# Kernel tuning notes

Hardware: AMD Instinct MI355X
Metric: run time of the kernel (lower is better)

The kernel has to match this reference:

```python
import jax, jax.numpy as jnp
import numpy as np

N_QUBITS = 12
LAYERS = 2
BATCH = 1024


def _apply_1q(state, gate, q):
    # state: [B] + [2]*n (wire 0 = leading qubit axis); gate: [2,2] or [B,2,2]
    axis = 1 + q
    st = jnp.moveaxis(state, axis, -1)
    if gate.ndim == 2:
        st = jnp.einsum('ij,...j->...i', gate, st)
    else:  # batched gate (angle depends on the input sample)
        st = jnp.einsum('bij,b...j->b...i', gate, st)
    return jnp.moveaxis(st, -1, axis)


def _apply_cnot(state, c, t):
    # flip target axis on the control=1 slice
    ca, ta = 1 + c, 1 + t
    a0 = jnp.take(state, 0, axis=ca)
    a1 = jnp.take(state, 1, axis=ca)
    ta2 = ta - 1 if ta > ca else ta
    a1 = jnp.flip(a1, axis=ta2)
    return jnp.stack([a0, a1], axis=ca)


def _rx(a):
    # a: [B] -> gate [B,2,2]
    h = 0.5 * a
    c = jnp.cos(h).astype(jnp.complex64)
    s = (-1j) * jnp.sin(h).astype(jnp.complex64)
    return jnp.stack([jnp.stack([c, s], -1), jnp.stack([s, c], -1)], -2)


def _ry(a):
    h = 0.5 * a
    c = jnp.cos(h).astype(jnp.complex64)
    s = jnp.sin(h).astype(jnp.complex64)
    return jnp.stack([jnp.stack([c, -s], -1), jnp.stack([s, c], -1)], -2)


def _rz(a):
    h = 0.5 * a
    e0 = jnp.exp(-1j * h.astype(jnp.complex64))
    e1 = jnp.exp(1j * h.astype(jnp.complex64))
    z = jnp.zeros_like(e0)
    return jnp.stack([jnp.stack([e0, z], -1), jnp.stack([z, e1], -1)], -2)


def setup_inputs() -> dict:
    key = jax.random.key(0)
    k1, k2 = jax.random.split(key)
    x = jax.random.normal(k1, (BATCH, N_QUBITS), dtype=jnp.float32)
    theta = jax.random.normal(k2, (LAYERS, N_QUBITS, 2), dtype=jnp.float32)
    lam = jnp.ones((LAYERS, N_QUBITS), dtype=jnp.float32)
    return {"x": x, "theta": theta, "lam": lam}


def reference(x, theta, lam):
    B = x.shape[0]
    n = N_QUBITS
    # |0...0> state, batched: [B] + [2]*n
    state = jnp.zeros((B,) + (2,) * n, dtype=jnp.complex64)
    state = state.at[(slice(None),) + (0,) * n].set(1.0)
    for l in range(LAYERS):
        for q in range(n):
            state = _apply_1q(state, _rx(lam[l, q] * x[:, q]), q)
        for q in range(n):
            state = _apply_cnot(state, q, (q + 1) % n)
        for q in range(n):
            state = _apply_1q(state, _ry(theta[l, q, 0]), q)
            state = _apply_1q(state, _rz(theta[l, q, 1]), q)
    probs = state.real ** 2 + state.imag ** 2  # [B] + [2]*n
    zs = []
    for q in range(n):
        axes = tuple(i for i in range(1, n + 1) if i != 1 + q)
        p = jnp.sum(probs, axis=axes)  # [B, 2]
        zs.append(p[:, 0] - p[:, 1])   # <Z_q>
    return jnp.stack(zs, axis=1)  # [B, n_qubits]
```

## Files before the change

### kernel.cpp

```cpp
#include <hip/hip_runtime.h>
#include <math.h>

#define NQ 12
#define TPB 256


__device__ __forceinline__ float2 pk_mul(float2 a, float2 b) {
    float2 d;
    asm("v_pk_mul_f32 %0, %1, %2" : "=v"(d) : "v"(a), "v"(b));
    return d;
}
__device__ __forceinline__ float2 pk_fma(float2 a, float2 b, float2 c) {
    float2 d;
    asm("v_pk_fma_f32 %0, %1, %2, %3" : "=v"(d) : "v"(a), "v"(b), "v"(c));
    return d;
}
__device__ __forceinline__ float2 pk_fma_sw0(float2 a, float2 b, float2 c) {
    float2 d;
    asm("v_pk_fma_f32 %0, %1, %2, %3 op_sel:[1,0,0] op_sel_hi:[0,1,1]"
        : "=v"(d) : "v"(a), "v"(b), "v"(c));
    return d;
}
__device__ __forceinline__ float2 pk_fma_n1(float2 a, float2 b, float2 c) {
    float2 d;
    asm("v_pk_fma_f32 %0, %1, %2, %3 neg_lo:[0,1,0] neg_hi:[0,1,0]"
        : "=v"(d) : "v"(a), "v"(b), "v"(c));
    return d;
}
__device__ __forceinline__ float2 pk_fma_sw0n1(float2 a, float2 b, float2 c) {
    float2 d;
    asm("v_pk_fma_f32 %0, %1, %2, %3 op_sel:[1,0,0] op_sel_hi:[0,1,1] "
        "neg_lo:[0,1,0] neg_hi:[0,1,0]"
        : "=v"(d) : "v"(a), "v"(b), "v"(c));
    return d;
}

#define FOR_PAIRS4(RB, ...) do {                                      \
    const int msk_ = 1 << (RB);                                       \
    _Pragma("unroll")                                                 \
    for (int h_ = 0; h_ < 8; ++h_) {                                  \
        const int i0 = ((h_ & ~(msk_ - 1)) << 1) | (h_ & (msk_ - 1)); \
        const int i1 = i0 | msk_;                                     \
        __VA_ARGS__;                                                  \
    } } while (0)

#define ADDR_A(r) (VA ^ (257 * (r)))
#define ADDR_B(r) (VB ^ (17 * (r)))
#define ADDR_C(r) (VC ^ (r))

#define LOCAL_X(AS, AD) do {                                          \
    _Pragma("unroll")                                                 \
    for (int r_ = 0; r_ < 16; ++r_) S[AS(r_)] = v[r_];                \
    _Pragma("unroll")                                                 \
    for (int r_ = 0; r_ < 16; ++r_) v[r_] = S[AD(r_)];                \
  } while (0)

#define M_GATE(q, RB) do {                                                  \
        const float2 ar = gm[q][0];                                         \
        const float2 ai = gm[q][1];                                         \
        const float2 br = gm[q][2];                                         \
        const float2 bi = gm[q][3];                                         \
        FOR_PAIRS4(RB,                                                      \
            const float2 v0 = v[i0];                                        \
            const float2 v1 = v[i1];                                        \
            float2 n0 = pk_mul(v0, ar);                                     \
            n0 = pk_fma_sw0(v0, ai, n0);                                    \
            n0 = pk_fma_n1(v1, br, n0);                                     \
            n0 = pk_fma_sw0(v1, bi, n0);                                    \
            float2 n1 = pk_mul(v0, br);                                     \
            n1 = pk_fma_sw0(v0, bi, n1);                                    \
            n1 = pk_fma(v1, ar, n1);                                        \
            n1 = pk_fma_sw0n1(v1, ai, n1);                                  \
            v[i0] = n0; v[i1] = n1;                                         \
        );                                                                  \
    } while (0)

#define RY_GATE(q, RB) do {                                                 \
        const float2 c2 = gy[q][0];                                         \
        const float2 s2 = gy[q][1];                                         \
        FOR_PAIRS4(RB,                                                      \
            float2 n0 = pk_fma_n1(v[i1], s2, pk_mul(v[i0], c2));            \
            float2 n1 = pk_fma(v[i0], s2, pk_mul(v[i1], c2));               \
            v[i0] = n0; v[i1] = n1;                                         \
        );                                                                  \
    } while (0)

#define M_PHASE(QB)  do { _Pragma("unroll")                                 \
    for (int d_ = 0; d_ < 4; ++d_) M_GATE((QB) + d_, 3 - d_); } while (0)
#define RY_PHASE(QB) do { _Pragma("unroll")                                 \
    for (int d_ = 0; d_ < 4; ++d_) RY_GATE((QB) + d_, 3 - d_); } while (0)

__global__ __launch_bounds__(TPB, 4) void vqc_kernel(
    const float* __restrict__ x,
    const float* __restrict__ th,
    const float* __restrict__ lm,
    float* __restrict__ out)
{
    __shared__ float2 S[4096];
    __shared__ float2 gm[12][4];
    __shared__ float2 gy[12][2];
    __shared__ float2 coI[12];
    __shared__ float red[4 * 12];

    const int b = blockIdx.x;
    const int t = threadIdx.x;
    const int l = t & 63;
    const int w = t >> 6;

    const int kC = (t ^ (t >> 4)) & 15;
    const int VA = (t & 0xF0) | kC;
    const int VB = ((t >> 4) << 8) | kC;
    const int VC = (t << 4) | kC;
    int Ft;
    {
        int yt = t ^ (t >> 1); yt ^= yt >> 2; yt ^= yt >> 4; yt ^= yt >> 8;
        int pt = (yt & 0x7FF) | ((__popc(t) & 1) << 11);
        Ft = (pt & ~15) | ((pt ^ (pt >> 4) ^ (pt >> 8)) & 15);
    }

    if (t < 12) {
        float h = 0.5f * lm[t] * x[b * NQ + t];
        float c, s; __sincosf(h, &s, &c);
        coI[t] = make_float2(c, s);
    } else if (t < 24) {
        int q = t - 12;
        float h = 0.5f * th[24 + 2 * q];
        float c, s; __sincosf(h, &s, &c);
        gy[q][0] = make_float2(c, c);
        gy[q][1] = make_float2(s, s);
    } else if (t < 36) {
        int q = t - 24;
        float ha = 0.5f * lm[12 + q] * x[b * NQ + q];
        float hy = 0.5f * th[2 * q];
        float hz = 0.5f * th[2 * q + 1];
        float ca, sa, cy, sy, cz, sz;
        __sincosf(ha, &sa, &ca);
        __sincosf(hy, &sy, &cy);
        __sincosf(hz, &sz, &cz);
        float ax = ca*cy*cz + sa*sy*sz;
        float ay = -(ca*cy*sz + sa*sy*cz);
        float bx = ca*sy*cz - sa*cy*sz;
        float by = ca*sy*sz - sa*cy*cz;
        gm[q][0] = make_float2(ax, ax);
        gm[q][1] = make_float2(-ay, ay);
        gm[q][2] = make_float2(bx, bx);
        gm[q][3] = make_float2(-by, by);
    }
    __syncthreads();

    float2 v[16];

    {
        const int g = (t ^ (t >> 1)) & 0x3F;
        float Pt = 1.0f;
#pragma unroll
        for (int m = 0; m < 6; ++m) {
            float2 cs = coI[7 - m];
            Pt *= ((g >> m) & 1) ? cs.y : cs.x;
        }
        const int ct = __popc(g);
        const int t0 = t & 1, t7 = (t >> 7) & 1;
        const int e1 = ((t >> 6) ^ (t >> 7)) & 1;
        float2 q11 = coI[11], q10 = coI[10], q9 = coI[9],
               q8 = coI[8], q1 = coI[1], q0 = coI[0];
        const float u8  = t0 ? q8.y : q8.x;
        const float u8n = t0 ? q8.x : q8.y;
        const float u1  = e1 ? q1.y : q1.x;
        const float u1n = e1 ? q1.x : q1.y;
        const float u0  = t7 ? q0.y : q0.x;
        const float u0n = t7 ? q0.x : q0.y;
#pragma unroll
        for (int r = 0; r < 16; ++r) {
            const int r0 = r & 1, r1 = (r >> 1) & 1, r2 = (r >> 2) & 1,
                      r3 = (r >> 3) & 1;
            const int b11 = r0 ^ r1, b10 = r1 ^ r2, b9 = r2 ^ r3;
            float m = Pt * (b11 ? q11.y : q11.x) * (b10 ? q10.y : q10.x)
                         * (b9 ? q9.y : q9.x) * (r3 ? u8n : u8)
                         * (r0 ? u1n : u1) * (r0 ? u0n : u0);
            int k = (ct + b11 + b10 + b9 + (r3 ^ t0) + (r0 ^ e1) + (r0 ^ t7)) & 3;
            v[r].x = (k == 0) ? m : ((k == 2) ? -m : 0.0f);
            v[r].y = (k == 3) ? m : ((k == 1) ? -m : 0.0f);
        }
    }

    M_PHASE(8);
    LOCAL_X(ADDR_C, ADDR_B);
    M_PHASE(4);
#pragma unroll
    for (int r = 0; r < 16; ++r) S[ADDR_B(r)] = v[r];
    __syncthreads();
#pragma unroll
    for (int r = 0; r < 16; ++r) v[r] = S[ADDR_A(r)];
    M_PHASE(0);

    __syncthreads();
#pragma unroll
    for (int r = 0; r < 16; ++r) {
        const int jr = r << 8;
        int yr = jr ^ (jr >> 1); yr ^= yr >> 2; yr ^= yr >> 4; yr ^= yr >> 8;
        const int pr = (yr & 0x7FF) | (((__popc(jr) ^ (jr >> 11)) & 1) << 11);
        const int Gr = (pr & ~15) | ((pr ^ (pr >> 4) ^ (pr >> 8)) & 15);
        S[Ft ^ Gr] = v[r];
    }
    __syncthreads();
#pragma unroll
    for (int r = 0; r < 16; ++r) v[r] = S[ADDR_A(r)];

    RY_PHASE(0);
#pragma unroll
    for (int r = 0; r < 16; ++r) S[ADDR_A(r)] = v[r];
    __syncthreads();
#pragma unroll
    for (int r = 0; r < 16; ++r) v[r] = S[ADDR_B(r)];
    RY_PHASE(4);
    LOCAL_X(ADDR_B, ADDR_C);
    RY_PHASE(8);

    float p[16];
#pragma unroll
    for (int r = 0; r < 16; ++r)
        p[r] = fmaf(v[r].x, v[r].x, v[r].y * v[r].y);
    float sA[8], dA[8];
#pragma unroll
    for (int k = 0; k < 8; ++k) {
        sA[k] = p[2 * k] + p[2 * k + 1];
        dA[k] = p[2 * k] - p[2 * k + 1];
    }
    float z11 = ((dA[0] + dA[1]) + (dA[2] + dA[3]))
              + ((dA[4] + dA[5]) + (dA[6] + dA[7]));
    float sC[4], dC[4];
#pragma unroll
    for (int k = 0; k < 4; ++k) {
        sC[k] = sA[2 * k] + sA[2 * k + 1];
        dC[k] = sA[2 * k] - sA[2 * k + 1];
    }
    float z10 = (dC[0] + dC[1]) + (dC[2] + dC[3]);
    float e0 = sC[0] + sC[1], f0 = sC[0] - sC[1];
    float e1s = sC[2] + sC[3], f1 = sC[2] - sC[3];
    float vals[5];
    vals[0] = e0 + e1s;
    vals[1] = e0 - e1s;
    vals[2] = f0 + f1;
    vals[3] = z10;
    vals[4] = z11;

#pragma unroll
    for (int k = 0; k < 6; ++k) {
        const float sgn = ((l >> k) & 1) ? -1.f : 1.f;
#pragma unroll
        for (int m = 0; m < 5; ++m) {
            float tmp = __shfl_xor(vals[m], 1 << k, 64);
            vals[m] = fmaf(sgn, vals[m], tmp);
        }
    }
    if (l == 0) {
        red[w * 12 + 0]  = vals[0];
        red[w * 12 + 8]  = vals[1];
        red[w * 12 + 9]  = vals[2];
        red[w * 12 + 10] = vals[3];
        red[w * 12 + 11] = vals[4];
    } else if (__popc(l) == 1) {
        int q = 8 - __ffs(l);
        red[w * 12 + q] = vals[0];
    }
    __syncthreads();
    if (t < NQ) {
        float acc = 0.f;
#pragma unroll
        for (int ww = 0; ww < 4; ++ww) {
            if (t < 2) {
                float pv = red[ww * 12 + 0];
                acc += ((ww >> (1 - t)) & 1) ? -pv : pv;
            } else {
                acc += red[ww * 12 + t];
            }
        }
        out[b * NQ + t] = acc;
    }
}

extern "C" void kernel_launch(void* const* d_in, const int* in_sizes, int n_in,
                              void* d_out, int out_size, void* d_ws, size_t ws_size,
                              hipStream_t stream) {
    const int B = in_sizes[0] / NQ;
    vqc_kernel<<<B, TPB, 0, stream>>>((const float*)d_in[0],
                                      (const float*)d_in[1],
                                      (const float*)d_in[2],
                                      (float*)d_out);
}
```

Baseline: 73.29 us.

## Redesign shared-memory state layout for 128-bit gathers in qubit transposes

Replaces the XOR-swizzled per-element shared-memory exchange with a new layout where each thread's 16 amplitudes come back as eight float4 (128-bit) LDS reads. Stores use new swizzled bases and the CNOT permutation mapping is rewritten to match. Gate coefficients are also loaded as float4, and the gate order within each phase is reversed to follow the new register-bit assignment. An extra __syncthreads is added before each cross-thread store because stores now overwrite data other threads may still be reading. This trades fewer LDS instructions for extra barriers and a possible rise in bank conflicts on the stores.

New measurement: 74.43 us. About the same (+1.5%).

```diff
diff --git a/kernel.cpp b/kernel.cpp
--- a/kernel.cpp
+++ b/kernel.cpp
@@ -44,22 +44,35 @@
         __VA_ARGS__;                                                  \
     } } while (0)
 
-#define ADDR_A(r) (VA ^ (257 * (r)))
-#define ADDR_B(r) (VB ^ (17 * (r)))
-#define ADDR_C(r) (VC ^ (r))
-
-#define LOCAL_X(AS, AD) do {                                          \
+#define GATHER do {                                                   \
     _Pragma("unroll")                                                 \
-    for (int r_ = 0; r_ < 16; ++r_) S[AS(r_)] = v[r_];                \
+    for (int k_ = 0; k_ < 8; ++k_) {                                  \
+        float4 g_ = F4[RB4 ^ k_];                                     \
+        v[2 * k_]     = make_float2(g_.x, g_.y);                      \
+        v[2 * k_ + 1] = make_float2(g_.z, g_.w);                      \
+    } } while (0)
+
+#define STORE_LOCAL do {                                              \
     _Pragma("unroll")                                                 \
-    for (int r_ = 0; r_ < 16; ++r_) v[r_] = S[AD(r_)];                \
-  } while (0)
+    for (int r_ = 0; r_ < 16; ++r_)                                   \
+        S[base1 ^ ((r_ << 4) | ((r_ & 7) << 1))] = v[r_];             \
+    } while (0)
+
+#define STORE_CROSS do {                                              \
+    _Pragma("unroll")                                                 \
+    for (int r_ = 0; r_ < 16; ++r_)                                   \
+        S[base2 + (r_ << 8)] = v[r_];                                 \
+    } while (0)
+
+#define CFENCE asm volatile("" ::: "memory")
 
 #define M_GATE(q, RB) do {                                                  \
-        const float2 ar = gm[q][0];                                         \
-        const float2 ai = gm[q][1];                                         \
-        const float2 br = gm[q][2];                                         \
-        const float2 bi = gm[q][3];                                         \
+        const float4 gA_ = gm4[2 * (q)];                                    \
+        const float4 gB_ = gm4[2 * (q) + 1];                                \
+        const float2 ar = make_float2(gA_.x, gA_.y);                        \
+        const float2 ai = make_float2(gA_.z, gA_.w);                        \
+        const float2 br = make_float2(gB_.x, gB_.y);                        \
+        const float2 bi = make_float2(gB_.z, gB_.w);                        \
         FOR_PAIRS4(RB,                                                      \
             const float2 v0 = v[i0];                                        \
             const float2 v1 = v[i1];                                        \
@@ -76,8 +89,9 @@
     } while (0)
 
 #define RY_GATE(q, RB) do {                                                 \
-        const float2 c2 = gy[q][0];                                         \
-        const float2 s2 = gy[q][1];                                         \
+        const float4 gY_ = gy4[q];                                          \
+        const float2 c2 = make_float2(gY_.x, gY_.y);                        \
+        const float2 s2 = make_float2(gY_.z, gY_.w);                        \
         FOR_PAIRS4(RB,                                                      \
             float2 n0 = pk_fma_n1(v[i1], s2, pk_mul(v[i0], c2));            \
             float2 n1 = pk_fma(v[i0], s2, pk_mul(v[i1], c2));               \
@@ -86,9 +100,9 @@
     } while (0)
 
 #define M_PHASE(QB)  do { _Pragma("unroll")                                 \
-    for (int d_ = 0; d_ < 4; ++d_) M_GATE((QB) + d_, 3 - d_); } while (0)
+    for (int d_ = 3; d_ >= 0; --d_) M_GATE((QB) + d_, 3 - d_); } while (0)
 #define RY_PHASE(QB) do { _Pragma("unroll")                                 \
-    for (int d_ = 0; d_ < 4; ++d_) RY_GATE((QB) + d_, 3 - d_); } while (0)
+    for (int d_ = 3; d_ >= 0; --d_) RY_GATE((QB) + d_, 3 - d_); } while (0)
 
 __global__ __launch_bounds__(TPB, 4) void vqc_kernel(
     const float* __restrict__ x,
@@ -96,26 +110,30 @@
     const float* __restrict__ lm,
     float* __restrict__ out)
 {
-    __shared__ float2 S[4096];
-    __shared__ float2 gm[12][4];
-    __shared__ float2 gy[12][2];
+    __shared__ alignas(16) float2 S[4096];
+    __shared__ alignas(16) float2 gm[12][4];
+    __shared__ alignas(16) float2 gy[12][2];
     __shared__ float2 coI[12];
     __shared__ float red[4 * 12];
+
+    float4* F4 = reinterpret_cast<float4*>(S);
+    const float4* gm4 = reinterpret_cast<const float4*>(gm);
+    const float4* gy4 = reinterpret_cast<const float4*>(gy);
 
     const int b = blockIdx.x;
     const int t = threadIdx.x;
     const int l = t & 63;
     const int w = t >> 6;
 
-    const int kC = (t ^ (t >> 4)) & 15;
-    const int VA = (t & 0xF0) | kC;
-    const int VB = ((t >> 4) << 8) | kC;
-    const int VC = (t << 4) | kC;
-    int Ft;
+    const int RB4   = (t << 3) | (t & 7);
+    const int base1 = ((t & 0xF0) << 4) | (t & 15);
+    const int base2 = ((t & 15) << 4)
+                    | ((((t >> 4) & 15) ^ ((t & 7) << 1)) & 15);
+    int Et3;
     {
         int yt = t ^ (t >> 1); yt ^= yt >> 2; yt ^= yt >> 4; yt ^= yt >> 8;
         int pt = (yt & 0x7FF) | ((__popc(t) & 1) << 11);
-        Ft = (pt & ~15) | ((pt ^ (pt >> 4) ^ (pt >> 8)) & 15);
+        Et3 = ((pt & 0xFF) << 4) | ((((pt >> 8) & 15) ^ ((pt & 7) << 1)) & 15);
     }
 
     if (t < 12) {
@@ -184,13 +202,12 @@
     }
 
     M_PHASE(8);
-    LOCAL_X(ADDR_C, ADDR_B);
+    STORE_LOCAL; CFENCE; GATHER;
     M_PHASE(4);
-#pragma unroll
-    for (int r = 0; r < 16; ++r) S[ADDR_B(r)] = v[r];
-    __syncthreads();
-#pragma unroll
-    for (int r = 0; r < 16; ++r) v[r] = S[ADDR_A(r)];
+    __syncthreads();
+    STORE_CROSS;
+    __syncthreads();
+    GATHER;
     M_PHASE(0);
 
     __syncthreads();
@@ -199,21 +216,20 @@
         const int jr = r << 8;
         int yr = jr ^ (jr >> 1); yr ^= yr >> 2; yr ^= yr >> 4; yr ^= yr >> 8;
         const int pr = (yr & 0x7FF) | (((__popc(jr) ^ (jr >> 11)) & 1) << 11);
-        const int Gr = (pr & ~15) | ((pr ^ (pr >> 4) ^ (pr >> 8)) & 15);
-        S[Ft ^ Gr] = v[r];
-    }
-    __syncthreads();
-#pragma unroll
-    for (int r = 0; r < 16; ++r) v[r] = S[ADDR_A(r)];
+        const int Gr = ((pr & 0xFF) << 4)
+                     | ((((pr >> 8) & 15) ^ ((pr & 7) << 1)) & 15);
+        S[Et3 ^ Gr] = v[r];
+    }
+    __syncthreads();
+    GATHER;
 
     RY_PHASE(0);
-#pragma unroll
-    for (int r = 0; r < 16; ++r) S[ADDR_A(r)] = v[r];
-    __syncthreads();
-#pragma unroll
-    for (int r = 0; r < 16; ++r) v[r] = S[ADDR_B(r)];
+    __syncthreads();
+    STORE_CROSS;
+    __syncthreads();
+    GATHER;
     RY_PHASE(4);
-    LOCAL_X(ADDR_B, ADDR_C);
+    STORE_LOCAL; CFENCE; GATHER;
     RY_PHASE(8);
 
     float p[16];
```

## Process two batch samples per block with interleaved state vectors

Applied to the files above, without the earlier changes.

Each block now simulates two samples at once, keeping two 16-amplitude register sets and two shared-memory state buffers, and interleaves their gate work. The aim is more instruction-level parallelism and fewer barriers per sample, at the cost of doubled registers and LDS per block, half as many blocks (512), and lower launch-bounds occupancy. Grid launch assumes an even batch size.

New measurement: 75.93 us. 1.04x slower.

```diff
diff --git a/kernel.cpp b/kernel.cpp
--- a/kernel.cpp
+++ b/kernel.cpp
@@ -48,64 +48,80 @@
 #define ADDR_B(r) (VB ^ (17 * (r)))
 #define ADDR_C(r) (VC ^ (r))
 
-#define LOCAL_X(AS, AD) do {                                          \
+#define CFENCE asm volatile("" ::: "memory")
+
+#define LOCAL_X2(AS, AD) do {                                         \
     _Pragma("unroll")                                                 \
-    for (int r_ = 0; r_ < 16; ++r_) S[AS(r_)] = v[r_];                \
+    for (int r_ = 0; r_ < 16; ++r_) {                                 \
+        S0[AS(r_)] = v0[r_]; S1[AS(r_)] = v1[r_];                     \
+    }                                                                 \
+    CFENCE;                                                           \
     _Pragma("unroll")                                                 \
-    for (int r_ = 0; r_ < 16; ++r_) v[r_] = S[AD(r_)];                \
-  } while (0)
-
-#define M_GATE(q, RB) do {                                                  \
-        const float2 ar = gm[q][0];                                         \
-        const float2 ai = gm[q][1];                                         \
-        const float2 br = gm[q][2];                                         \
-        const float2 bi = gm[q][3];                                         \
+    for (int r_ = 0; r_ < 16; ++r_) {                                 \
+        v0[r_] = S0[AD(r_)]; v1[r_] = S1[AD(r_)];                     \
+    } } while (0)
+
+#define M_GATE(GM, q, RB, V) do {                                           \
+        const float2 ar = GM[q][0];                                         \
+        const float2 ai = GM[q][1];                                         \
+        const float2 br = GM[q][2];                                         \
+        const float2 bi = GM[q][3];                                         \
         FOR_PAIRS4(RB,                                                      \
-            const float2 v0 = v[i0];                                        \
-            const float2 v1 = v[i1];                                        \
-            float2 n0 = pk_mul(v0, ar);                                     \
-            n0 = pk_fma_sw0(v0, ai, n0);                                    \
-            n0 = pk_fma_n1(v1, br, n0);                                     \
-            n0 = pk_fma_sw0(v1, bi, n0);                                    \
-            float2 n1 = pk_mul(v0, br);                                     \
-            n1 = pk_fma_sw0(v0, bi, n1);                                    \
-            n1 = pk_fma(v1, ar, n1);                                        \
-            n1 = pk_fma_sw0n1(v1, ai, n1);                                  \
-            v[i0] = n0; v[i1] = n1;                                         \
+            const float2 a0 = V[i0];                                        \
+            const float2 a1 = V[i1];                                        \
+            float2 n0 = pk_mul(a0, ar);                                     \
+            n0 = pk_fma_sw0(a0, ai, n0);                                    \
+            n0 = pk_fma_n1(a1, br, n0);                                     \
+            n0 = pk_fma_sw0(a1, bi, n0);                                    \
+            float2 n1 = pk_mul(a0, br);                                     \
+            n1 = pk_fma_sw0(a0, bi, n1);                                    \
+            n1 = pk_fma(a1, ar, n1);                                        \
+            n1 = pk_fma_sw0n1(a1, ai, n1);                                  \
+            V[i0] = n0; V[i1] = n1;                                         \
         );                                                                  \
     } while (0)
 
-#define RY_GATE(q, RB) do {                                                 \
+#define RY_GATE(q, RB, V) do {                                              \
         const float2 c2 = gy[q][0];                                         \
         const float2 s2 = gy[q][1];                                         \
         FOR_PAIRS4(RB,                                                      \
-            float2 n0 = pk_fma_n1(v[i1], s2, pk_mul(v[i0], c2));            \
-            float2 n1 = pk_fma(v[i0], s2, pk_mul(v[i1], c2));               \
-            v[i0] = n0; v[i1] = n1;                                         \
+            float2 n0 = pk_fma_n1(V[i1], s2, pk_mul(V[i0], c2));            \
+            float2 n1 = pk_fma(V[i0], s2, pk_mul(V[i1], c2));               \
+            V[i0] = n0; V[i1] = n1;                                         \
         );                                                                  \
     } while (0)
 
-#define M_PHASE(QB)  do { _Pragma("unroll")                                 \
-    for (int d_ = 0; d_ < 4; ++d_) M_GATE((QB) + d_, 3 - d_); } while (0)
-#define RY_PHASE(QB) do { _Pragma("unroll")                                 \
-    for (int d_ = 0; d_ < 4; ++d_) RY_GATE((QB) + d_, 3 - d_); } while (0)
-
-__global__ __launch_bounds__(TPB, 4) void vqc_kernel(
+#define M_PHASE2(QB)  do { _Pragma("unroll")                                \
+    for (int d_ = 0; d_ < 4; ++d_) {                                        \
+        M_GATE(gmP0, (QB) + d_, 3 - d_, v0);                                \
+        M_GATE(gmP1, (QB) + d_, 3 - d_, v1);                                \
+    } } while (0)
+#define RY_PHASE2(QB) do { _Pragma("unroll")                                \
+    for (int d_ = 0; d_ < 4; ++d_) {                                        \
+        RY_GATE((QB) + d_, 3 - d_, v0);                                     \
+        RY_GATE((QB) + d_, 3 - d_, v1);                                     \
+    } } while (0)
+
+__global__ __launch_bounds__(TPB, 2) void vqc_kernel(
     const float* __restrict__ x,
     const float* __restrict__ th,
     const float* __restrict__ lm,
     float* __restrict__ out)
 {
-    __shared__ float2 S[4096];
-    __shared__ float2 gm[12][4];
+    __shared__ alignas(16) float2 S0[4096];
+    __shared__ alignas(16) float2 S1[4096];
+    __shared__ float2 gm[2][12][4];
     __shared__ float2 gy[12][2];
-    __shared__ float2 coI[12];
-    __shared__ float red[4 * 12];
+    __shared__ float2 coI[2][12];
+    __shared__ float red[2][4 * 12];
 
     const int b = blockIdx.x;
     const int t = threadIdx.x;
     const int l = t & 63;
     const int w = t >> 6;
+
+    const float2 (*gmP0)[4] = gm[0];
+    const float2 (*gmP1)[4] = gm[1];
 
     const int kC = (t ^ (t >> 4)) & 15;
     const int VA = (t & 0xF0) | kC;
@@ -118,51 +134,58 @@
         Ft = (pt & ~15) | ((pt ^ (pt >> 4) ^ (pt >> 8)) & 15);
     }
 
-    if (t < 12) {
-        float h = 0.5f * lm[t] * x[b * NQ + t];
-        float c, s; __sincosf(h, &s, &c);
-        coI[t] = make_float2(c, s);
-    } else if (t < 24) {
-        int q = t - 12;
-        float h = 0.5f * th[24 + 2 * q];
-        float c, s; __sincosf(h, &s, &c);
-        gy[q][0] = make_float2(c, c);
-        gy[q][1] = make_float2(s, s);
-    } else if (t < 36) {
-        int q = t - 24;
-        float ha = 0.5f * lm[12 + q] * x[b * NQ + q];
-        float hy = 0.5f * th[2 * q];
-        float hz = 0.5f * th[2 * q + 1];
-        float ca, sa, cy, sy, cz, sz;
-        __sincosf(ha, &sa, &ca);
-        __sincosf(hy, &sy, &cy);
-        __sincosf(hz, &sz, &cz);
-        float ax = ca*cy*cz + sa*sy*sz;
-        float ay = -(ca*cy*sz + sa*sy*cz);
-        float bx = ca*sy*cz - sa*cy*sz;
-        float by = ca*sy*sz - sa*cy*cz;
-        gm[q][0] = make_float2(ax, ax);
-        gm[q][1] = make_float2(-ay, ay);
-        gm[q][2] = make_float2(bx, bx);
-        gm[q][3] = make_float2(-by, by);
-    }
-    __syncthreads();
-
-    float2 v[16];
-
-    {
+    if (t < 72) {
+        const int s = t / 36;
+        const int u = t - 36 * s;
+        const int bb = 2 * b + s;
+        if (u < 12) {
+            float h = 0.5f * lm[u] * x[bb * NQ + u];
+            float c, sn; __sincosf(h, &sn, &c);
+            coI[s][u] = make_float2(c, sn);
+        } else if (u < 24) {
+            if (s == 0) {
+                int q = u - 12;
+                float h = 0.5f * th[24 + 2 * q];
+                float c, sn; __sincosf(h, &sn, &c);
+                gy[q][0] = make_float2(c, c);
+                gy[q][1] = make_float2(sn, sn);
+            }
+        } else {
+            int q = u - 24;
+            float ha = 0.5f * lm[12 + q] * x[bb * NQ + q];
+            float hy = 0.5f * th[2 * q];
+            float hz = 0.5f * th[2 * q + 1];
+            float ca, sa, cy, sy, cz, sz;
+            __sincosf(ha, &sa, &ca);
+            __sincosf(hy, &sy, &cy);
+            __sincosf(hz, &sz, &cz);
+            float ax = ca*cy*cz + sa*sy*sz;
+            float ay = -(ca*cy*sz + sa*sy*cz);
+            float bx = ca*sy*cz - sa*cy*sz;
+            float by = ca*sy*sz - sa*cy*cz;
+            gm[s][q][0] = make_float2(ax, ax);
+            gm[s][q][1] = make_float2(-ay, ay);
+            gm[s][q][2] = make_float2(bx, bx);
+            gm[s][q][3] = make_float2(-by, by);
+        }
+    }
+    __syncthreads();
+
+    float2 v0[16], v1[16];
+
+    auto init_state = [&](const float2* coIs, float2* v) {
         const int g = (t ^ (t >> 1)) & 0x3F;
         float Pt = 1.0f;
 #pragma unroll
         for (int m = 0; m < 6; ++m) {
-            float2 cs = coI[7 - m];
+            float2 cs = coIs[7 - m];
             Pt *= ((g >> m) & 1) ? cs.y : cs.x;
         }
         const int ct = __popc(g);
         const int t0 = t & 1, t7 = (t >> 7) & 1;
         const int e1 = ((t >> 6) ^ (t >> 7)) & 1;
-        float2 q11 = coI[11], q10 = coI[10], q9 = coI[9],
-               q8 = coI[8], q1 = coI[1], q0 = coI[0];
+        float2 q11 = coIs[11], q10 = coIs[10], q9 = coIs[9],
+               q8 = coIs[8], q1 = coIs[1], q0 = coIs[0];
         const float u8  = t0 ? q8.y : q8.x;
         const float u8n = t0 ? q8.x : q8.y;
         const float u1  = e1 ? q1.y : q1.x;
@@ -181,17 +204,23 @@
             v[r].x = (k == 0) ? m : ((k == 2) ? -m : 0.0f);
             v[r].y = (k == 3) ? m : ((k == 1) ? -m : 0.0f);
         }
-    }
-
-    M_PHASE(8);
-    LOCAL_X(ADDR_C, ADDR_B);
-    M_PHASE(4);
-#pragma unroll
-    for (int r = 0; r < 16; ++r) S[ADDR_B(r)] = v[r];
-    __syncthreads();
-#pragma unroll
-    for (int r = 0; r < 16; ++r) v[r] = S[ADDR_A(r)];
-    M_PHASE(0);
+    };
+    init_state(coI[0], v0);
+    init_state(coI[1], v1);
+
+    M_PHASE2(8);
+    LOCAL_X2(ADDR_C, ADDR_B);
+    M_PHASE2(4);
+#pragma unroll
+    for (int r = 0; r < 16; ++r) {
+        S0[ADDR_B(r)] = v0[r]; S1[ADDR_B(r)] = v1[r];
+    }
+    __syncthreads();
+#pragma unroll
+    for (int r = 0; r < 16; ++r) {
+        v0[r] = S0[ADDR_A(r)]; v1[r] = S1[ADDR_A(r)];
+    }
+    M_PHASE2(0);
 
     __syncthreads();
 #pragma unroll
@@ -200,82 +229,98 @@
         int yr = jr ^ (jr >> 1); yr ^= yr >> 2; yr ^= yr >> 4; yr ^= yr >> 8;
         const int pr = (yr & 0x7FF) | (((__popc(jr) ^ (jr >> 11)) & 1) << 11);
         const int Gr = (pr & ~15) | ((pr ^ (pr >> 4) ^ (pr >> 8)) & 15);
-        S[Ft ^ Gr] = v[r];
-    }
-    __syncthreads();
-#pragma unroll
-    for (int r = 0; r < 16; ++r) v[r] = S[ADDR_A(r)];
-
-    RY_PHASE(0);
-#pragma unroll
-    for (int r = 0; r < 16; ++r) S[ADDR_A(r)] = v[r];
-    __syncthreads();
-#pragma unroll
-    for (int r = 0; r < 16; ++r) v[r] = S[ADDR_B(r)];
-    RY_PHASE(4);
-    LOCAL_X(ADDR_B, ADDR_C);
-    RY_PHASE(8);
-
-    float p[16];
-#pragma unroll
-    for (int r = 0; r < 16; ++r)
-        p[r] = fmaf(v[r].x, v[r].x, v[r].y * v[r].y);
-    float sA[8], dA[8];
-#pragma unroll
-    for (int k = 0; k < 8; ++k) {
-        sA[k] = p[2 * k] + p[2 * k + 1];
-        dA[k] = p[2 * k] - p[2 * k + 1];
-    }
-    float z11 = ((dA[0] + dA[1]) + (dA[2] + dA[3]))
-              + ((dA[4] + dA[5]) + (dA[6] + dA[7]));
-    float sC[4], dC[4];
-#pragma unroll
-    for (int k = 0; k < 4; ++k) {
-        sC[k] = sA[2 * k] + sA[2 * k + 1];
-        dC[k] = sA[2 * k] - sA[2 * k + 1];
-    }
-    float z10 = (dC[0] + dC[1]) + (dC[2] + dC[3]);
-    float e0 = sC[0] + sC[1], f0 = sC[0] - sC[1];
-    float e1s = sC[2] + sC[3], f1 = sC[2] - sC[3];
-    float vals[5];
-    vals[0] = e0 + e1s;
-    vals[1] = e0 - e1s;
-    vals[2] = f0 + f1;
-    vals[3] = z10;
-    vals[4] = z11;
+        S0[Ft ^ Gr] = v0[r]; S1[Ft ^ Gr] = v1[r];
+    }
+    __syncthreads();
+#pragma unroll
+    for (int r = 0; r < 16; ++r) {
+        v0[r] = S0[ADDR_A(r)]; v1[r] = S1[ADDR_A(r)];
+    }
+
+    RY_PHASE2(0);
+#pragma unroll
+    for (int r = 0; r < 16; ++r) {
+        S0[ADDR_A(r)] = v0[r]; S1[ADDR_A(r)] = v1[r];
+    }
+    __syncthreads();
+#pragma unroll
+    for (int r = 0; r < 16; ++r) {
+        v0[r] = S0[ADDR_B(r)]; v1[r] = S1[ADDR_B(r)];
+    }
+    RY_PHASE2(4);
+    LOCAL_X2(ADDR_B, ADDR_C);
+    RY_PHASE2(8);
+
+    float vals[10];
+    auto reduce5 = [&](const float2* v, float* va) {
+        float p[16];
+#pragma unroll
+        for (int r = 0; r < 16; ++r)
+            p[r] = fmaf(v[r].x, v[r].x, v[r].y * v[r].y);
+        float sA[8], dA[8];
+#pragma unroll
+        for (int k = 0; k < 8; ++k) {
+            sA[k] = p[2 * k] + p[2 * k + 1];
+            dA[k] = p[2 * k] - p[2 * k + 1];
+        }
+        float z11 = ((dA[0] + dA[1]) + (dA[2] + dA[3]))
+                  + ((dA[4] + dA[5]) + (dA[6] + dA[7]));
+        float sC[4], dC[4];
+#pragma unroll
+        for (int k = 0; k < 4; ++k) {
+            sC[k] = sA[2 * k] + sA[2 * k + 1];
+            dC[k] = sA[2 * k] - sA[2 * k + 1];
+        }
+        float z10 = (dC[0] + dC[1]) + (dC[2] + dC[3]);
+        float e0 = sC[0] + sC[1], f0 = sC[0] - sC[1];
+        float e1s = sC[2] + sC[3], f1 = sC[2] - sC[3];
+        va[0] = e0 + e1s;
+        va[1] = e0 - e1s;
+        va[2] = f0 + f1;
+        va[3] = z10;
+        va[4] = z11;
+    };
+    reduce5(v0, vals);
+    reduce5(v1, vals + 5);
 
 #pragma unroll
     for (int k = 0; k < 6; ++k) {
         const float sgn = ((l >> k) & 1) ? -1.f : 1.f;
 #pragma unroll
-        for (int m = 0; m < 5; ++m) {
+        for (int m = 0; m < 10; ++m) {
             float tmp = __shfl_xor(vals[m], 1 << k, 64);
             vals[m] = fmaf(sgn, vals[m], tmp);
         }
     }
     if (l == 0) {
-        red[w * 12 + 0]  = vals[0];
-        red[w * 12 + 8]  = vals[1];
-        red[w * 12 + 9]  = vals[2];
-        red[w * 12 + 10] = vals[3];
-        red[w * 12 + 11] = vals[4];
+#pragma unroll
+        for (int s = 0; s < 2; ++s) {
+            red[s][w * 12 + 0]  = vals[5 * s + 0];
+            red[s][w * 12 + 8]  = vals[5 * s + 1];
+            red[s][w * 12 + 9]  = vals[5 * s + 2];
+            red[s][w * 12 + 10] = vals[5 * s + 3];
+            red[s][w * 12 + 11] = vals[5 * s + 4];
+        }
     } else if (__popc(l) == 1) {
         int q = 8 - __ffs(l);
-        red[w * 12 + q] = vals[0];
-    }
-    __syncthreads();
-    if (t < NQ) {
+        red[0][w * 12 + q] = vals[0];
+        red[1][w * 12 + q] = vals[5];
+    }
+    __syncthreads();
+    if (t < 2 * NQ) {
+        const int s = t / NQ;
+        const int q = t - NQ * s;
         float acc = 0.f;
 #pragma unroll
         for (int ww = 0; ww < 4; ++ww) {
-            if (t < 2) {
-                float pv = red[ww * 12 + 0];
-                acc += ((ww >> (1 - t)) & 1) ? -pv : pv;
+            if (q < 2) {
+                float pv = red[s][ww * 12 + 0];
+                acc += ((ww >> (1 - q)) & 1) ? -pv : pv;
             } else {
-                acc += red[ww * 12 + t];
+                acc += red[s][ww * 12 + q];
             }
         }
-        out[b * NQ + t] = acc;
+        out[(2 * b + s) * NQ + q] = acc;
     }
 }
 
@@ -283,8 +328,8 @@
                               void* d_out, int out_size, void* d_ws, size_t ws_size,
                               hipStream_t stream) {
     const int B = in_sizes[0] / NQ;
-    vqc_kernel<<<B, TPB, 0, stream>>>((const float*)d_in[0],
-                                      (const float*)d_in[1],
-                                      (const float*)d_in[2],
-                                      (float*)d_out);
-}
+    vqc_kernel<<<B / 2, TPB, 0, stream>>>((const float*)d_in[0],
+                                          (const float*)d_in[1],
+                                          (const float*)d_in[2],
+                                          (float*)d_out);
+}
```

## Process four batch samples per block in a loop

Applied to the files above, without the earlier changes.

Each block now loops over four batch samples, and the launch uses a quarter as many blocks. This amortises block launch overhead and reuses the resident block across samples. It also adds a compiler memory fence inside the local shared-memory exchange and renames temporaries in the gate macro. The trade-off is fewer blocks: 256 blocks on 256 CUs leaves roughly one block per CU with no latency hiding, and each sample is processed serially. Sample loads and trig setup are not overlapped with the previous sample's compute. B is also assumed to be divisible by 4.

New measurement: 94.48 us. 1.29x slower.

```diff
diff --git a/kernel.cpp b/kernel.cpp
--- a/kernel.cpp
+++ b/kernel.cpp
@@ -48,9 +48,12 @@
 #define ADDR_B(r) (VB ^ (17 * (r)))
 #define ADDR_C(r) (VC ^ (r))
 
+#define CFENCE asm volatile("" ::: "memory")
+
 #define LOCAL_X(AS, AD) do {                                          \
     _Pragma("unroll")                                                 \
     for (int r_ = 0; r_ < 16; ++r_) S[AS(r_)] = v[r_];                \
+    CFENCE;                                                           \
     _Pragma("unroll")                                                 \
     for (int r_ = 0; r_ < 16; ++r_) v[r_] = S[AD(r_)];                \
   } while (0)
@@ -61,16 +64,16 @@
         const float2 br = gm[q][2];                                         \
         const float2 bi = gm[q][3];                                         \
         FOR_PAIRS4(RB,                                                      \
-            const float2 v0 = v[i0];                                        \
-            const float2 v1 = v[i1];                                        \
-            float2 n0 = pk_mul(v0, ar);                                     \
-            n0 = pk_fma_sw0(v0, ai, n0);                                    \
-            n0 = pk_fma_n1(v1, br, n0);                                     \
-            n0 = pk_fma_sw0(v1, bi, n0);                                    \
-            float2 n1 = pk_mul(v0, br);                                     \
-            n1 = pk_fma_sw0(v0, bi, n1);                                    \
-            n1 = pk_fma(v1, ar, n1);                                        \
-            n1 = pk_fma_sw0n1(v1, ai, n1);                                  \
+            const float2 a0 = v[i0];                                        \
+            const float2 a1 = v[i1];                                        \
+            float2 n0 = pk_mul(a0, ar);                                     \
+            n0 = pk_fma_sw0(a0, ai, n0);                                    \
+            n0 = pk_fma_n1(a1, br, n0);                                     \
+            n0 = pk_fma_sw0(a1, bi, n0);                                    \
+            float2 n1 = pk_mul(a0, br);                                     \
+            n1 = pk_fma_sw0(a0, bi, n1);                                    \
+            n1 = pk_fma(a1, ar, n1);                                        \
+            n1 = pk_fma_sw0n1(a1, ai, n1);                                  \
             v[i0] = n0; v[i1] = n1;                                         \
         );                                                                  \
     } while (0)
@@ -102,7 +105,6 @@
     __shared__ float2 coI[12];
     __shared__ float red[4 * 12];
 
-    const int b = blockIdx.x;
     const int t = threadIdx.x;
     const int l = t & 63;
     const int w = t >> 6;
@@ -118,164 +120,169 @@
         Ft = (pt & ~15) | ((pt ^ (pt >> 4) ^ (pt >> 8)) & 15);
     }
 
-    if (t < 12) {
-        float h = 0.5f * lm[t] * x[b * NQ + t];
-        float c, s; __sincosf(h, &s, &c);
-        coI[t] = make_float2(c, s);
-    } else if (t < 24) {
-        int q = t - 12;
-        float h = 0.5f * th[24 + 2 * q];
-        float c, s; __sincosf(h, &s, &c);
-        gy[q][0] = make_float2(c, c);
-        gy[q][1] = make_float2(s, s);
-    } else if (t < 36) {
-        int q = t - 24;
-        float ha = 0.5f * lm[12 + q] * x[b * NQ + q];
-        float hy = 0.5f * th[2 * q];
-        float hz = 0.5f * th[2 * q + 1];
-        float ca, sa, cy, sy, cz, sz;
-        __sincosf(ha, &sa, &ca);
-        __sincosf(hy, &sy, &cy);
-        __sincosf(hz, &sz, &cz);
-        float ax = ca*cy*cz + sa*sy*sz;
-        float ay = -(ca*cy*sz + sa*sy*cz);
-        float bx = ca*sy*cz - sa*cy*sz;
-        float by = ca*sy*sz - sa*cy*cz;
-        gm[q][0] = make_float2(ax, ax);
-        gm[q][1] = make_float2(-ay, ay);
-        gm[q][2] = make_float2(bx, bx);
-        gm[q][3] = make_float2(-by, by);
-    }
-    __syncthreads();
-
-    float2 v[16];
-
-    {
-        const int g = (t ^ (t >> 1)) & 0x3F;
-        float Pt = 1.0f;
-#pragma unroll
-        for (int m = 0; m < 6; ++m) {
-            float2 cs = coI[7 - m];
-            Pt *= ((g >> m) & 1) ? cs.y : cs.x;
-        }
-        const int ct = __popc(g);
-        const int t0 = t & 1, t7 = (t >> 7) & 1;
-        const int e1 = ((t >> 6) ^ (t >> 7)) & 1;
-        float2 q11 = coI[11], q10 = coI[10], q9 = coI[9],
-               q8 = coI[8], q1 = coI[1], q0 = coI[0];
-        const float u8  = t0 ? q8.y : q8.x;
-        const float u8n = t0 ? q8.x : q8.y;
-        const float u1  = e1 ? q1.y : q1.x;
-        const float u1n = e1 ? q1.x : q1.y;
-        const float u0  = t7 ? q0.y : q0.x;
-        const float u0n = t7 ? q0.x : q0.y;
+    for (int s = 0; s < 4; ++s) {
+        const int b = blockIdx.x * 4 + s;
+
+        if (t < 12) {
+            float h = 0.5f * lm[t] * x[b * NQ + t];
+            float c, sn; __sincosf(h, &sn, &c);
+            coI[t] = make_float2(c, sn);
+        } else if (t < 24) {
+            int q = t - 12;
+            float h = 0.5f * th[24 + 2 * q];
+            float c, sn; __sincosf(h, &sn, &c);
+            gy[q][0] = make_float2(c, c);
+            gy[q][1] = make_float2(sn, sn);
+        } else if (t < 36) {
+            int q = t - 24;
+            float ha = 0.5f * lm[12 + q] * x[b * NQ + q];
+            float hy = 0.5f * th[2 * q];
+            float hz = 0.5f * th[2 * q + 1];
+            float ca, sa, cy, sy, cz, sz;
+            __sincosf(ha, &sa, &ca);
+            __sincosf(hy, &sy, &cy);
+            __sincosf(hz, &sz, &cz);
+            float ax = ca*cy*cz + sa*sy*sz;
+            float ay = -(ca*cy*sz + sa*sy*cz);
+            float bx = ca*sy*cz - sa*cy*sz;
+            float by = ca*sy*sz - sa*cy*cz;
+            gm[q][0] = make_float2(ax, ax);
+            gm[q][1] = make_float2(-ay, ay);
+            gm[q][2] = make_float2(bx, bx);
+            gm[q][3] = make_float2(-by, by);
+        }
+        __syncthreads();
+
+        float2 v[16];
+
+        {
+            const int g = (t ^ (t >> 1)) & 0x3F;
+            float Pt = 1.0f;
+#pragma unroll
+            for (int m = 0; m < 6; ++m) {
+                float2 cs = coI[7 - m];
+                Pt *= ((g >> m) & 1) ? cs.y : cs.x;
+            }
+            const int ct = __popc(g);
+            const int t0 = t & 1, t7 = (t >> 7) & 1;
+            const int e1 = ((t >> 6) ^ (t >> 7)) & 1;
+            float2 q11 = coI[11], q10 = coI[10], q9 = coI[9],
+                   q8 = coI[8], q1 = coI[1], q0 = coI[0];
+            const float u8  = t0 ? q8.y : q8.x;
+            const float u8n = t0 ? q8.x : q8.y;
+            const float u1  = e1 ? q1.y : q1.x;
+            const float u1n = e1 ? q1.x : q1.y;
+            const float u0  = t7 ? q0.y : q0.x;
+            const float u0n = t7 ? q0.x : q0.y;
+#pragma unroll
+            for (int r = 0; r < 16; ++r) {
+                const int r0 = r & 1, r1 = (r >> 1) & 1, r2 = (r >> 2) & 1,
+                          r3 = (r >> 3) & 1;
+                const int b11 = r0 ^ r1, b10 = r1 ^ r2, b9 = r2 ^ r3;
+                float m = Pt * (b11 ? q11.y : q11.x) * (b10 ? q10.y : q10.x)
+                             * (b9 ? q9.y : q9.x) * (r3 ? u8n : u8)
+                             * (r0 ? u1n : u1) * (r0 ? u0n : u0);
+                int k = (ct + b11 + b10 + b9 + (r3 ^ t0) + (r0 ^ e1) + (r0 ^ t7)) & 3;
+                v[r].x = (k == 0) ? m : ((k == 2) ? -m : 0.0f);
+                v[r].y = (k == 3) ? m : ((k == 1) ? -m : 0.0f);
+            }
+        }
+
+        M_PHASE(8);
+        LOCAL_X(ADDR_C, ADDR_B);
+        M_PHASE(4);
+#pragma unroll
+        for (int r = 0; r < 16; ++r) S[ADDR_B(r)] = v[r];
+        __syncthreads();
+#pragma unroll
+        for (int r = 0; r < 16; ++r) v[r] = S[ADDR_A(r)];
+        M_PHASE(0);
+
+        __syncthreads();
 #pragma unroll
         for (int r = 0; r < 16; ++r) {
-            const int r0 = r & 1, r1 = (r >> 1) & 1, r2 = (r >> 2) & 1,
-                      r3 = (r >> 3) & 1;
-            const int b11 = r0 ^ r1, b10 = r1 ^ r2, b9 = r2 ^ r3;
-            float m = Pt * (b11 ? q11.y : q11.x) * (b10 ? q10.y : q10.x)
-                         * (b9 ? q9.y : q9.x) * (r3 ? u8n : u8)
-                         * (r0 ? u1n : u1) * (r0 ? u0n : u0);
-            int k = (ct + b11 + b10 + b9 + (r3 ^ t0) + (r0 ^ e1) + (r0 ^ t7)) & 3;
-            v[r].x = (k == 0) ? m : ((k == 2) ? -m : 0.0f);
-            v[r].y = (k == 3) ? m : ((k == 1) ? -m : 0.0f);
-        }
-    }
-
-    M_PHASE(8);
-    LOCAL_X(ADDR_C, ADDR_B);
-    M_PHASE(4);
-#pragma unroll
-    for (int r = 0; r < 16; ++r) S[ADDR_B(r)] = v[r];
-    __syncthreads();
-#pragma unroll
-    for (int r = 0; r < 16; ++r) v[r] = S[ADDR_A(r)];
-    M_PHASE(0);
-
-    __syncthreads();
-#pragma unroll
-    for (int r = 0; r < 16; ++r) {
-        const int jr = r << 8;
-        int yr = jr ^ (jr >> 1); yr ^= yr >> 2; yr ^= yr >> 4; yr ^= yr >> 8;
-        const int pr = (yr & 0x7FF) | (((__popc(jr) ^ (jr >> 11)) & 1) << 11);
-        const int Gr = (pr & ~15) | ((pr ^ (pr >> 4) ^ (pr >> 8)) & 15);
-        S[Ft ^ Gr] = v[r];
-    }
-    __syncthreads();
-#pragma unroll
-    for (int r = 0; r < 16; ++r) v[r] = S[ADDR_A(r)];
-
-    RY_PHASE(0);
-#pragma unroll
-    for (int r = 0; r < 16; ++r) S[ADDR_A(r)] = v[r];
-    __syncthreads();
-#pragma unroll
-    for (int r = 0; r < 16; ++r) v[r] = S[ADDR_B(r)];
-    RY_PHASE(4);
-    LOCAL_X(ADDR_B, ADDR_C);
-    RY_PHASE(8);
-
-    float p[16];
-#pragma unroll
-    for (int r = 0; r < 16; ++r)
-        p[r] = fmaf(v[r].x, v[r].x, v[r].y * v[r].y);
-    float sA[8], dA[8];
-#pragma unroll
-    for (int k = 0; k < 8; ++k) {
-        sA[k] = p[2 * k] + p[2 * k + 1];
-        dA[k] = p[2 * k] - p[2 * k + 1];
-    }
-    float z11 = ((dA[0] + dA[1]) + (dA[2] + dA[3]))
-              + ((dA[4] + dA[5]) + (dA[6] + dA[7]));
-    float sC[4], dC[4];
-#pragma unroll
-    for (int k = 0; k < 4; ++k) {
-        sC[k] = sA[2 * k] + sA[2 * k + 1];
-        dC[k] = sA[2 * k] - sA[2 * k + 1];
-    }
-    float z10 = (dC[0] + dC[1]) + (dC[2] + dC[3]);
-    float e0 = sC[0] + sC[1], f0 = sC[0] - sC[1];
-    float e1s = sC[2] + sC[3], f1 = sC[2] - sC[3];
-    float vals[5];
-    vals[0] = e0 + e1s;
-    vals[1] = e0 - e1s;
-    vals[2] = f0 + f1;
-    vals[3] = z10;
-    vals[4] = z11;
-
-#pragma unroll
-    for (int k = 0; k < 6; ++k) {
-        const float sgn = ((l >> k) & 1) ? -1.f : 1.f;
-#pragma unroll
-        for (int m = 0; m < 5; ++m) {
-            float tmp = __shfl_xor(vals[m], 1 << k, 64);
-            vals[m] = fmaf(sgn, vals[m], tmp);
-        }
-    }
-    if (l == 0) {
-        red[w * 12 + 0]  = vals[0];
-        red[w * 12 + 8]  = vals[1];
-        red[w * 12 + 9]  = vals[2];
-        red[w * 12 + 10] = vals[3];
-        red[w * 12 + 11] = vals[4];
-    } else if (__popc(l) == 1) {
-        int q = 8 - __ffs(l);
-        red[w * 12 + q] = vals[0];
-    }
-    __syncthreads();
-    if (t < NQ) {
-        float acc = 0.f;
-#pragma unroll
-        for (int ww = 0; ww < 4; ++ww) {
-            if (t < 2) {
-                float pv = red[ww * 12 + 0];
-                acc += ((ww >> (1 - t)) & 1) ? -pv : pv;
-            } else {
-                acc += red[ww * 12 + t];
-            }
-        }
-        out[b * NQ + t] = acc;
+            const int jr = r << 8;
+            int yr = jr ^ (jr >> 1); yr ^= yr >> 2; yr ^= yr >> 4; yr ^= yr >> 8;
+            const int pr = (yr & 0x7FF) | (((__popc(jr) ^ (jr >> 11)) & 1) << 11);
+            const int Gr = (pr & ~15) | ((pr ^ (pr >> 4) ^ (pr >> 8)) & 15);
+            S[Ft ^ Gr] = v[r];
+        }
+        __syncthreads();
+#pragma unroll
+        for (int r = 0; r < 16; ++r) v[r] = S[ADDR_A(r)];
+
+        RY_PHASE(0);
+#pragma unroll
+        for (int r = 0; r < 16; ++r) S[ADDR_A(r)] = v[r];
+        __syncthreads();
+#pragma unroll
+        for (int r = 0; r < 16; ++r) v[r] = S[ADDR_B(r)];
+        RY_PHASE(4);
+        LOCAL_X(ADDR_B, ADDR_C);
+        RY_PHASE(8);
+
+        float p[16];
+#pragma unroll
+        for (int r = 0; r < 16; ++r)
+            p[r] = fmaf(v[r].x, v[r].x, v[r].y * v[r].y);
+        float sA[8], dA[8];
+#pragma unroll
+        for (int k = 0; k < 8; ++k) {
+            sA[k] = p[2 * k] + p[2 * k + 1];
+            dA[k] = p[2 * k] - p[2 * k + 1];
+        }
+        float z11 = ((dA[0] + dA[1]) + (dA[2] + dA[3]))
+                  + ((dA[4] + dA[5]) + (dA[6] + dA[7]));
+        float sC[4], dC[4];
+#pragma unroll
+        for (int k = 0; k < 4; ++k) {
+            sC[k] = sA[2 * k] + sA[2 * k + 1];
+            dC[k] = sA[2 * k] - sA[2 * k + 1];
+        }
+        float z10 = (dC[0] + dC[1]) + (dC[2] + dC[3]);
+        float e0 = sC[0] + sC[1], f0 = sC[0] - sC[1];
+        float e1s = sC[2] + sC[3], f1 = sC[2] - sC[3];
+        float vals[5];
+        vals[0] = e0 + e1s;
+        vals[1] = e0 - e1s;
+        vals[2] = f0 + f1;
+        vals[3] = z10;
+        vals[4] = z11;
+
+#pragma unroll
+        for (int k = 0; k < 6; ++k) {
+            const float sgn = ((l >> k) & 1) ? -1.f : 1.f;
+#pragma unroll
+            for (int m = 0; m < 5; ++m) {
+                float tmp = __shfl_xor(vals[m], 1 << k, 64);
+                vals[m] = fmaf(sgn, vals[m], tmp);
+            }
+        }
+        if (l == 0) {
+            red[w * 12 + 0]  = vals[0];
+            red[w * 12 + 8]  = vals[1];
+            red[w * 12 + 9]  = vals[2];
+            red[w * 12 + 10] = vals[3];
+            red[w * 12 + 11] = vals[4];
+        } else if (__popc(l) == 1) {
+            int q = 8 - __ffs(l);
+            red[w * 12 + q] = vals[0];
+        }
+        __syncthreads();
+        if (t < NQ) {
+            float acc = 0.f;
+#pragma unroll
+            for (int ww = 0; ww < 4; ++ww) {
+                if (t < 2) {
+                    float pv = red[ww * 12 + 0];
+                    acc += ((ww >> (1 - t)) & 1) ? -pv : pv;
+                } else {
+                    acc += red[ww * 12 + t];
+                }
+            }
+            out[b * NQ + t] = acc;
+        }
+        __syncthreads();
     }
 }
 
@@ -283,8 +290,8 @@
                               void* d_out, int out_size, void* d_ws, size_t ws_size,
                               hipStream_t stream) {
     const int B = in_sizes[0] / NQ;
-    vqc_kernel<<<B, TPB, 0, stream>>>((const float*)d_in[0],
-                                      (const float*)d_in[1],
-                                      (const float*)d_in[2],
-                                      (float*)d_out);
-}
+    vqc_kernel<<<B / 4, TPB, 0, stream>>>((const float*)d_in[0],
+                                          (const float*)d_in[1],
+                                          (const float*)d_in[2],
+                                          (float*)d_out);
+}
```
